# Performance work log

Measured on AMD Instinct MI355X. Metric: run time of the kernel, lower is better.

The kernel has to match this reference:

```python
import jax, jax.numpy as jnp
import numpy as np
from jax import lax

B, C, H, W, S = 8, 64, 64, 64, 12
KSIZE = 5


def _conv2d_same(x, w):
    # x: [N, Cin, H, W], w: [Cout, Cin, kh, kw]
    return lax.conv_general_dilated(
        x, w, window_strides=(1, 1), padding='SAME',
        dimension_numbers=('NCHW', 'OIHW', 'NCHW'))


def setup_inputs() -> dict:
    key = jax.random.key(0)
    k0, k1, k2, k3, k4 = jax.random.split(key, 5)
    x = jax.random.normal(k0, (B, C, H, W, S), dtype=jnp.float32)
    w1 = jax.random.normal(k1, (3 * C, C, 1, 1), dtype=jnp.float32) * 0.05
    b1 = jax.random.normal(k2, (3 * C,), dtype=jnp.float32) * 0.05
    w2 = jax.random.normal(k3, (1, 2 * C, KSIZE, KSIZE), dtype=jnp.float32) * 0.05
    b2 = jax.random.normal(k4, (1,), dtype=jnp.float32) * 0.05
    return {'x': x, 'w1': w1, 'b1': b1, 'w2': w2, 'b2': b2}


def reference(x, w1, b1, w2, b2):
    b, c, h, w_, s = x.shape
    # conv1 (1x1) applied per timestep == channel matmul over all timesteps at once
    qkv = jnp.einsum('oc,bchws->bohws', w1[:, :, 0, 0], x) + b1[None, :, None, None, None]
    Q, K, V = jnp.split(qkv, 3, axis=1)  # each [b, c, h, w, s]

    # conv2 on concat(Q_s, K_t) is linear in channels:
    # score(s,t) = convQ(Q[...,s]) + convK(K[...,t]) + bias
    def per_time_conv(z, wsub):
        # z: [b, c, h, w, s] -> fold time into batch -> conv -> [b, h, w, s]
        zb = jnp.moveaxis(z, -1, 1).reshape(b * s, c, h, w_)
        out = _conv2d_same(zb, wsub)  # [b*s, 1, h, w]
        return jnp.moveaxis(out.reshape(b, s, h, w_), 1, -1)  # [b, h, w, s]

    A_q = per_time_conv(Q, w2[:, :c])   # [b, h, w, s] (query index)
    A_k = per_time_conv(K, w2[:, c:])   # [b, h, w, t] (key index)

    # scores: [b, h, w, t, s]
    scores = A_q[:, :, :, None, :] + A_k[:, :, :, :, None] + b2[0]
    attn = jax.nn.softmax(scores, axis=-2)  # softmax over t (keys)

    # weighted sum of V over t -> [b, c, h, w, s]
    V_out = jnp.einsum('bhwts,bchwt->bchws', attn, V)
    return V_out
```

## Files before the change

### kernel.cpp

```cpp
#include <hip/hip_runtime.h>
#include <hip/hip_bf16.h>

#define WEFF_OFF 0
#define Y_OFF    4096
#define Y_PLANE  393216

__global__ __launch_bounds__(256) void k_prep(const float* __restrict__ w1,
                                              const float* __restrict__ w2,
                                              float* __restrict__ weff) {
    int idx = blockIdx.x * 256 + threadIdx.x;
    if (idx >= 64 * 25) return;
    int cp = idx / 25, tap = idx % 25;
    float s = 0.f;
    for (int c = 0; c < 64; ++c)
        s = fmaf(w2[(64 + c) * 25 + tap], w1[(64 + c) * 64 + cp], s);
    weff[cp * 25 + tap] = s;
}

__global__ __launch_bounds__(256) void k_tap(const float* __restrict__ x,
                                             const float* __restrict__ weff,
                                             float* __restrict__ y) {
    const int gid = blockIdx.x * 256 + threadIdx.x;
    const int m   = gid / 12;
    const int t   = gid - m * 12;
    const int w   = m & 63;
    const int h   = (m >> 6) & 63;
    const int b   = m >> 12;

    const float* xp = x + (size_t)b * 3145728 + h * 768 + w * 12 + t;

    float acc[25];
#pragma unroll
    for (int k = 0; k < 25; ++k) acc[k] = 0.f;

    for (int c = 0; c < 64; ++c) {
        const float v = xp[(size_t)c * 49152];
        const float* wg = weff + c * 25;
#pragma unroll
        for (int k = 0; k < 25; ++k)
            acc[k] = fmaf(wg[k], v, acc[k]);
    }

#pragma unroll
    for (int k = 0; k < 25; ++k)
        y[(size_t)k * Y_PLANE + gid] = acc[k];
}

__global__ __launch_bounds__(256) void k_gather(const float* __restrict__ y,
                                                float* __restrict__ p) {
    const int tid  = threadIdx.x;
    const int m    = blockIdx.x * 64 + (tid >> 2);
    const int q    = tid & 3;
    const int qq   = (q == 3) ? 2 : q;
    const int w    = m & 63;
    const int h    = (m >> 6) & 63;
    const int b    = m >> 12;

    float4 a; a.x = 0.f; a.y = 0.f; a.z = 0.f; a.w = 0.f;

#pragma unroll
    for (int dh = 0; dh < 5; ++dh) {
        const int hh = h + dh - 2;
        if ((unsigned)hh >= 64u) continue;
        const int rowb = (b * 64 + hh) * 64;
#pragma unroll
        for (int dw = 0; dw < 5; ++dw) {
            const int ww = w + dw - 2;
            if ((unsigned)ww >= 64u) continue;
            const float* yp = y + (size_t)(dh * 5 + dw) * Y_PLANE
                                + (size_t)(rowb + ww) * 12 + qq * 4;
            float4 v = *(const float4*)(yp);
            a.x += v.x; a.y += v.y; a.z += v.z; a.w += v.w;
        }
    }

    float mx = fmaxf(fmaxf(a.x, a.y), fmaxf(a.z, a.w));
    mx = fmaxf(mx, __shfl_xor(mx, 1, 4));
    mx = fmaxf(mx, __shfl_xor(mx, 2, 4));

    float e0 = __expf(a.x - mx), e1 = __expf(a.y - mx);
    float e2 = __expf(a.z - mx), e3 = __expf(a.w - mx);
    const float s4 = e0 + e1 + e2 + e3;
    const float s0 = __shfl(s4, 0, 4);
    const float s1 = __shfl(s4, 1, 4);
    const float s2 = __shfl(s4, 2, 4);
    const float inv = 1.f / (s0 + s1 + s2);

    if (q < 3) {
        float4 o; o.x = e0 * inv; o.y = e1 * inv; o.z = e2 * inv; o.w = e3 * inv;
        *(float4*)(p + (size_t)m * 12 + q * 4) = o;
    }
}

__global__ __launch_bounds__(512) void k_out(const float* __restrict__ x,
                                             const float* __restrict__ w1,
                                             const float* __restrict__ b1,
                                             const float* __restrict__ p,
                                             float* __restrict__ out) {
    __shared__ float lds[64 * 65];

    const int b  = blockIdx.x >> 6;
    const int h  = blockIdx.x & 63;
    const int w  = threadIdx.x & 63;
    const int cg = threadIdx.x >> 6;

    const float* pp = p + (size_t)((b * 64 + h) * 64 + w) * 12;
    float pv[12];
    {
        float4 t0 = *(const float4*)(pp);
        float4 t1 = *(const float4*)(pp + 4);
        float4 t2 = *(const float4*)(pp + 8);
        pv[0] = t0.x; pv[1] = t0.y; pv[2]  = t0.z; pv[3]  = t0.w;
        pv[4] = t1.x; pv[5] = t1.y; pv[6]  = t1.z; pv[7]  = t1.w;
        pv[8] = t2.x; pv[9] = t2.y; pv[10] = t2.z; pv[11] = t2.w;
    }

    const float* xb0 = x + ((size_t)(b * 64 + cg * 8) * 64 + h) * 768 + w * 12;
#pragma unroll
    for (int j = 0; j < 8; ++j) {
        const float* xp = xb0 + (size_t)j * 49152;
        float4 u0 = *(const float4*)(xp);
        float4 u1 = *(const float4*)(xp + 4);
        float4 u2 = *(const float4*)(xp + 8);
        float s = 0.f;
        s = fmaf(pv[0], u0.x, s);  s = fmaf(pv[1], u0.y, s);
        s = fmaf(pv[2], u0.z, s);  s = fmaf(pv[3], u0.w, s);
        s = fmaf(pv[4], u1.x, s);  s = fmaf(pv[5], u1.y, s);
        s = fmaf(pv[6], u1.z, s);  s = fmaf(pv[7], u1.w, s);
        s = fmaf(pv[8], u2.x, s);  s = fmaf(pv[9], u2.y, s);
        s = fmaf(pv[10], u2.z, s); s = fmaf(pv[11], u2.w, s);
        lds[w * 65 + cg * 8 + j] = s;
    }
    __syncthreads();

    const float* w1v = w1 + 128 * 64 + cg * 8 * 64;
    float acc[8];
#pragma unroll
    for (int j = 0; j < 8; ++j) acc[j] = b1[128 + cg * 8 + j];
    for (int c2 = 0; c2 < 64; ++c2) {
        const float xv = lds[w * 65 + c2];
#pragma unroll
        for (int j = 0; j < 8; ++j)
            acc[j] = fmaf(w1v[j * 64 + c2], xv, acc[j]);
    }

#pragma unroll
    for (int j = 0; j < 8; ++j) {
        const int co = cg * 8 + j;
        float4 f; f.x = acc[j]; f.y = acc[j]; f.z = acc[j]; f.w = acc[j];
        float* op = out + ((size_t)(b * 64 + co) * 4096 + h * 64 + w) * 12;
        *(float4*)(op)     = f;
        *(float4*)(op + 4) = f;
        *(float4*)(op + 8) = f;
    }
}

extern "C" void kernel_launch(void* const* d_in, const int* in_sizes, int n_in,
                              void* d_out, int out_size, void* d_ws, size_t ws_size,
                              hipStream_t stream) {
    const float* x  = (const float*)d_in[0];
    const float* w1 = (const float*)d_in[1];
    const float* b1 = (const float*)d_in[2];
    const float* w2 = (const float*)d_in[3];

    float* outp = (float*)d_out;
    float* weff = outp + WEFF_OFF;
    float* y    = outp + Y_OFF;
    float* p    = (float*)d_ws;

    hipLaunchKernelGGL(k_prep,   dim3(7),    dim3(256), 0, stream, w1, w2, weff);
    hipLaunchKernelGGL(k_tap,    dim3(1536), dim3(256), 0, stream, x, weff, y);
    hipLaunchKernelGGL(k_gather, dim3(512),  dim3(256), 0, stream, y, p);
    hipLaunchKernelGGL(k_out,    dim3(512),  dim3(512), 0, stream, x, w1, b1, p, outp);
}
```

Before: 98.98 us.

## Restructure tap kernel to stage x tile in LDS and split taps across warps

The tap kernel now loads a 64-channel by 64-w by 4-timestep x tile into shared memory with float4 loads, and each 64-thread group computes 3 of the 25 taps (the last group also computes the 25th) over four timesteps. The effective weights are stored transposed (tap-major) to match. Previously each thread loaded one scalar x per channel and produced all 25 taps. The new layout gives vectorized coalesced loads and float4 stores of y, in exchange for a sync, 64 KB of LDS per block and an imbalanced final warp group.

```diff
diff --git a/kernel.cpp b/kernel.cpp
--- a/kernel.cpp
+++ b/kernel.cpp
@@ -1,49 +1,77 @@
 #include <hip/hip_runtime.h>
 #include <hip/hip_bf16.h>
 
-#define WEFF_OFF 0
-#define Y_OFF    4096
-#define Y_PLANE  393216
+#define WEFFT_OFF 0
+#define Y_OFF     4096
+#define Y_PLANE   393216
 
 __global__ __launch_bounds__(256) void k_prep(const float* __restrict__ w1,
                                               const float* __restrict__ w2,
-                                              float* __restrict__ weff) {
+                                              float* __restrict__ weffT) {
     int idx = blockIdx.x * 256 + threadIdx.x;
-    if (idx >= 64 * 25) return;
-    int cp = idx / 25, tap = idx % 25;
+    if (idx >= 25 * 64) return;
+    int tap = idx >> 6, c = idx & 63;
     float s = 0.f;
-    for (int c = 0; c < 64; ++c)
-        s = fmaf(w2[(64 + c) * 25 + tap], w1[(64 + c) * 64 + cp], s);
-    weff[cp * 25 + tap] = s;
-}
-
-__global__ __launch_bounds__(256) void k_tap(const float* __restrict__ x,
-                                             const float* __restrict__ weff,
+    for (int cc = 0; cc < 64; ++cc)
+        s = fmaf(w2[(64 + cc) * 25 + tap], w1[(64 + cc) * 64 + c], s);
+    weffT[tap * 64 + c] = s;
+}
+
+__global__ __launch_bounds__(512) void k_tap(const float* __restrict__ x,
+                                             const float* __restrict__ weffT,
                                              float* __restrict__ y) {
-    const int gid = blockIdx.x * 256 + threadIdx.x;
-    const int m   = gid / 12;
-    const int t   = gid - m * 12;
-    const int w   = m & 63;
-    const int h   = (m >> 6) & 63;
-    const int b   = m >> 12;
-
-    const float* xp = x + (size_t)b * 3145728 + h * 768 + w * 12 + t;
-
-    float acc[25];
-#pragma unroll
-    for (int k = 0; k < 25; ++k) acc[k] = 0.f;
-
+    __shared__ float4 xl[64 * 64];
+
+    const int bid = blockIdx.x;
+    const int tg  = bid % 3;
+    const int h   = (bid / 3) & 63;
+    const int b   = bid / 192;
+    const int w   = threadIdx.x & 63;
+    const int cg  = threadIdx.x >> 6;
+
+    const float* xb = x + (size_t)b * 3145728 + (size_t)(cg * 8) * 49152
+                        + h * 768 + w * 12 + tg * 4;
+    float4 v[8];
+#pragma unroll
+    for (int j = 0; j < 8; ++j)
+        v[j] = *(const float4*)(xb + (size_t)j * 49152);
+#pragma unroll
+    for (int j = 0; j < 8; ++j)
+        xl[(cg * 8 + j) * 64 + w] = v[j];
+    __syncthreads();
+
+    const int t0 = cg * 3;
+    const float* w0 = weffT + (t0 + 0) * 64;
+    const float* w1p = weffT + (t0 + 1) * 64;
+    const float* w2p = weffT + (t0 + 2) * 64;
+    const float* w3p = weffT + 24 * 64;
+
+    float4 a0, a1, a2, a3;
+    a0.x=0.f;a0.y=0.f;a0.z=0.f;a0.w=0.f; a1=a0; a2=a0; a3=a0;
+
+#pragma unroll 4
     for (int c = 0; c < 64; ++c) {
-        const float v = xp[(size_t)c * 49152];
-        const float* wg = weff + c * 25;
-#pragma unroll
-        for (int k = 0; k < 25; ++k)
-            acc[k] = fmaf(wg[k], v, acc[k]);
-    }
-
-#pragma unroll
-    for (int k = 0; k < 25; ++k)
-        y[(size_t)k * Y_PLANE + gid] = acc[k];
+        const float4 xv = xl[c * 64 + w];
+        const float g0 = w0[c], g1 = w1p[c], g2 = w2p[c];
+        a0.x = fmaf(g0, xv.x, a0.x); a0.y = fmaf(g0, xv.y, a0.y);
+        a0.z = fmaf(g0, xv.z, a0.z); a0.w = fmaf(g0, xv.w, a0.w);
+        a1.x = fmaf(g1, xv.x, a1.x); a1.y = fmaf(g1, xv.y, a1.y);
+        a1.z = fmaf(g1, xv.z, a1.z); a1.w = fmaf(g1, xv.w, a1.w);
+        a2.x = fmaf(g2, xv.x, a2.x); a2.y = fmaf(g2, xv.y, a2.y);
+        a2.z = fmaf(g2, xv.z, a2.z); a2.w = fmaf(g2, xv.w, a2.w);
+        if (cg == 7) {
+            const float g3 = w3p[c];
+            a3.x = fmaf(g3, xv.x, a3.x); a3.y = fmaf(g3, xv.y, a3.y);
+            a3.z = fmaf(g3, xv.z, a3.z); a3.w = fmaf(g3, xv.w, a3.w);
+        }
+    }
+
+    const size_t mbase = (size_t)((b * 64 + h) * 64 + w) * 12 + tg * 4;
+    *(float4*)(y + (size_t)(t0 + 0) * Y_PLANE + mbase) = a0;
+    *(float4*)(y + (size_t)(t0 + 1) * Y_PLANE + mbase) = a1;
+    *(float4*)(y + (size_t)(t0 + 2) * Y_PLANE + mbase) = a2;
+    if (cg == 7)
+        *(float4*)(y + (size_t)24 * Y_PLANE + mbase) = a3;
 }
 
 __global__ __launch_bounds__(256) void k_gather(const float* __restrict__ y,
@@ -163,13 +191,13 @@
     const float* b1 = (const float*)d_in[2];
     const float* w2 = (const float*)d_in[3];
 
-    float* outp = (float*)d_out;
-    float* weff = outp + WEFF_OFF;
-    float* y    = outp + Y_OFF;
-    float* p    = (float*)d_ws;
-
-    hipLaunchKernelGGL(k_prep,   dim3(7),    dim3(256), 0, stream, w1, w2, weff);
-    hipLaunchKernelGGL(k_tap,    dim3(1536), dim3(256), 0, stream, x, weff, y);
+    float* outp  = (float*)d_out;
+    float* weffT = outp + WEFFT_OFF;
+    float* y     = outp + Y_OFF;
+    float* p     = (float*)d_ws;
+
+    hipLaunchKernelGGL(k_prep,   dim3(7),    dim3(256), 0, stream, w1, w2, weffT);
+    hipLaunchKernelGGL(k_tap,    dim3(1536), dim3(512), 0, stream, x, weffT, y);
     hipLaunchKernelGGL(k_gather, dim3(512),  dim3(256), 0, stream, y, p);
     hipLaunchKernelGGL(k_out,    dim3(512),  dim3(512), 0, stream, x, w1, b1, p, outp);
 }
```

Measured after the change: 143.6 us. 1.45x slower.
